# Kernel tuning notes

Measured on AMD Instinct MI355X. Metric: run time of the kernel, lower is better.

Reference implementation:

```python
import jax, jax.numpy as jnp
import numpy as np

B, H, S, E = 16384, 16, 1, 64
N_OTHERS = 4


def setup_inputs() -> dict:
    key = jax.random.key(0)
    ks = jax.random.split(key, N_OTHERS + 2)
    inp = {f"others_{i}": jax.random.normal(ks[i], (B, H, S, E), dtype=jnp.float32)
           for i in range(N_OTHERS)}
    inp["main"] = jax.random.normal(ks[N_OTHERS], (B, H, S, E), dtype=jnp.float32)
    inp["W"] = jax.random.normal(ks[N_OTHERS + 1], (E, E), dtype=jnp.float32) * (1.0 / np.sqrt(E))
    return inp


def reference(others_0, others_1, others_2, others_3, main, W):
    # mean over the 'others' modalities: (B, H, 1, E)
    mean = (others_0 + others_1 + others_2 + others_3) / 4.0
    m = jnp.squeeze(mean, 2)        # (B, H, E)
    main_sq = jnp.squeeze(main, 2)  # (B, H, E)
    # bilinear score: mean @ W @ main^T -> (B, H, H)
    score = jnp.einsum('bhe,ef,bgf->bhg', m, W, main_sq)
    attn = jax.nn.softmax(score, axis=-1)      # (B, H, H)
    context = jnp.einsum('bhg,bge->bhe', attn, main_sq)  # (B, H, E)
    return context, attn
```

## Files before the change

### kernel.cpp

```cpp
#include <hip/hip_runtime.h>

#define NBATCH 16384
#define H 16
#define E 64
#define NWAVE 4
#define NBLK (NBATCH / NWAVE)

typedef __attribute__((ext_vector_type(8))) short short8v;
typedef __attribute__((ext_vector_type(4))) float f32x4;

#define CFENCE asm volatile("" ::: "memory")

__device__ __forceinline__ unsigned short f2bf(float x) {
    return (unsigned short)(__float_as_uint(x) >> 16);
}
__device__ __forceinline__ float bfres(float x) {
    return x - __uint_as_float(__float_as_uint(x) & 0xFFFF0000u);
}

#define BSPLIT8(HIv, LOv, A, B) do { \
    HIv[0]=(short)f2bf(A.x); LOv[0]=(short)f2bf(bfres(A.x)); \
    HIv[1]=(short)f2bf(A.y); LOv[1]=(short)f2bf(bfres(A.y)); \
    HIv[2]=(short)f2bf(A.z); LOv[2]=(short)f2bf(bfres(A.z)); \
    HIv[3]=(short)f2bf(A.w); LOv[3]=(short)f2bf(bfres(A.w)); \
    HIv[4]=(short)f2bf(B.x); LOv[4]=(short)f2bf(bfres(B.x)); \
    HIv[5]=(short)f2bf(B.y); LOv[5]=(short)f2bf(bfres(B.y)); \
    HIv[6]=(short)f2bf(B.z); LOv[6]=(short)f2bf(bfres(B.z)); \
    HIv[7]=(short)f2bf(B.w); LOv[7]=(short)f2bf(bfres(B.w)); \
} while (0)

#define FMA4(ACC, S, B) do { \
    ACC.x = fmaf(S, B.x, ACC.x); ACC.y = fmaf(S, B.y, ACC.y); \
    ACC.z = fmaf(S, B.z, ACC.z); ACC.w = fmaf(S, B.w, ACC.w); } while (0)

#define SMAX1(X, OUT) do { \
    float mx_ = (X); \
    mx_ = fmaxf(mx_, __shfl_xor(mx_, 1)); \
    mx_ = fmaxf(mx_, __shfl_xor(mx_, 2)); \
    mx_ = fmaxf(mx_, __shfl_xor(mx_, 4)); \
    mx_ = fmaxf(mx_, __shfl_xor(mx_, 8)); \
    float e_ = __expf((X) - mx_); \
    float sm_ = e_; \
    sm_ += __shfl_xor(sm_, 1); \
    sm_ += __shfl_xor(sm_, 2); \
    sm_ += __shfl_xor(sm_, 4); \
    sm_ += __shfl_xor(sm_, 8); \
    OUT = e_ * __builtin_amdgcn_rcpf(sm_); \
} while (0)

__global__ __launch_bounds__(256) void w_frag_init(
    const float* __restrict__ W, unsigned short* __restrict__ wsW)
{
    const int flat = blockIdx.x * 256 + threadIdx.x;
    if (flat >= E * E) return;
    const float w = W[flat];
    const int e = flat >> 6, f = flat & 63;
    const int t = f >> 4, col = f & 15;
    const int s = e >> 5, khi = (e >> 3) & 3, i = e & 7;
    const int L = col + 16 * khi;
    wsW[((t * 2 + s) * 2 + 0) * 512 + L * 8 + i] = f2bf(w);
    wsW[((t * 2 + s) * 2 + 1) * 512 + L * 8 + i] = f2bf(bfres(w));
}

__global__ __launch_bounds__(256) void ovo_kernel(
    const float* __restrict__ o0, const float* __restrict__ o1,
    const float* __restrict__ o2, const float* __restrict__ o3,
    const float* __restrict__ mn, const unsigned short* __restrict__ wsW,
    float* __restrict__ ctx_out, float* __restrict__ attn_out)
{
    __shared__ float sT[NWAVE][2][H * 68];

    const int tid = threadIdx.x;
    const int l   = tid & 63;
    const int wv  = tid >> 6;
    const int r   = l & 15;
    const int q   = l >> 4;

    const int batch = blockIdx.x * NWAVE + wv;
    const size_t base = (size_t)batch * (H * E);

    float* const sU    = &sT[wv][0][0];
    float* const sMain = &sT[wv][1][0];

    float4 po0[4], po1[4], po2[4], po3[4];
#pragma unroll
    for (int sc = 0; sc < 4; ++sc) {
        const int s = sc >> 1, c01 = sc & 1;
        const size_t off = base + r * 64 + 32 * s + 8 * q + 4 * c01;
        po0[sc] = *(const float4*)(o0 + off);
        po1[sc] = *(const float4*)(o1 + off);
        po2[sc] = *(const float4*)(o2 + off);
        po3[sc] = *(const float4*)(o3 + off);
    }

    short8v ahi[2], alo[2];
#pragma unroll
    for (int s = 0; s < 2; ++s) {
        const int sa = s * 2, sb = s * 2 + 1;
        float4 mA, mB;
        mA.x = ((po0[sa].x + po1[sa].x) + (po2[sa].x + po3[sa].x)) * 0.25f;
        mA.y = ((po0[sa].y + po1[sa].y) + (po2[sa].y + po3[sa].y)) * 0.25f;
        mA.z = ((po0[sa].z + po1[sa].z) + (po2[sa].z + po3[sa].z)) * 0.25f;
        mA.w = ((po0[sa].w + po1[sa].w) + (po2[sa].w + po3[sa].w)) * 0.25f;
        mB.x = ((po0[sb].x + po1[sb].x) + (po2[sb].x + po3[sb].x)) * 0.25f;
        mB.y = ((po0[sb].y + po1[sb].y) + (po2[sb].y + po3[sb].y)) * 0.25f;
        mB.z = ((po0[sb].z + po1[sb].z) + (po2[sb].z + po3[sb].z)) * 0.25f;
        mB.w = ((po0[sb].w + po1[sb].w) + (po2[sb].w + po3[sb].w)) * 0.25f;
        BSPLIT8(ahi[s], alo[s], mA, mB);
    }

    float4 pmA, pmB, pmC, pmD;
    pmA = *(const float4*)(mn + base + r * 64 +      8 * q);
    pmB = *(const float4*)(mn + base + r * 64 +      8 * q + 4);
    pmC = *(const float4*)(mn + base + r * 64 + 32 + 8 * q);
    pmD = *(const float4*)(mn + base + r * 64 + 32 + 8 * q + 4);
    CFENCE;

#pragma unroll
    for (int t = 0; t < 4; ++t) {
        short8v bh0 = *(const short8v*)&wsW[((t * 2 + 0) * 2 + 0) * 512 + l * 8];
        short8v bl0 = *(const short8v*)&wsW[((t * 2 + 0) * 2 + 1) * 512 + l * 8];
        short8v bh1 = *(const short8v*)&wsW[((t * 2 + 1) * 2 + 0) * 512 + l * 8];
        short8v bl1 = *(const short8v*)&wsW[((t * 2 + 1) * 2 + 1) * 512 + l * 8];
        f32x4 acc = {0.f, 0.f, 0.f, 0.f};
        acc = __builtin_amdgcn_mfma_f32_16x16x32_bf16(ahi[0], bh0, acc, 0, 0, 0);
        acc = __builtin_amdgcn_mfma_f32_16x16x32_bf16(alo[0], bh0, acc, 0, 0, 0);
        acc = __builtin_amdgcn_mfma_f32_16x16x32_bf16(ahi[0], bl0, acc, 0, 0, 0);
        acc = __builtin_amdgcn_mfma_f32_16x16x32_bf16(ahi[1], bh1, acc, 0, 0, 0);
        acc = __builtin_amdgcn_mfma_f32_16x16x32_bf16(alo[1], bh1, acc, 0, 0, 0);
        acc = __builtin_amdgcn_mfma_f32_16x16x32_bf16(ahi[1], bl1, acc, 0, 0, 0);
#pragma unroll
        for (int j = 0; j < 4; ++j)
            sU[(4 * q + j) * 68 + 16 * t + r] = acc[j];
    }

    *(float4*)&sMain[r * 68 +      8 * q]     = pmA;
    *(float4*)&sMain[r * 68 +      8 * q + 4] = pmB;
    *(float4*)&sMain[r * 68 + 32 + 8 * q]     = pmC;
    *(float4*)&sMain[r * 68 + 32 + 8 * q + 4] = pmD;
    CFENCE;

    f32x4 d3 = {0.f, 0.f, 0.f, 0.f};
    {
        float4 a01 = *(const float4*)&sU[r * 68 + 8 * q];
        float4 a23 = *(const float4*)&sU[r * 68 + 8 * q + 4];
        short8v ah, al2, bh, bl2;
        BSPLIT8(ah, al2, a01, a23);
        BSPLIT8(bh, bl2, pmA, pmB);
        d3 = __builtin_amdgcn_mfma_f32_16x16x32_bf16(ah,  bh,  d3, 0, 0, 0);
        d3 = __builtin_amdgcn_mfma_f32_16x16x32_bf16(al2, bh,  d3, 0, 0, 0);
        d3 = __builtin_amdgcn_mfma_f32_16x16x32_bf16(ah,  bl2, d3, 0, 0, 0);
    }
    {
        float4 a01 = *(const float4*)&sU[r * 68 + 32 + 8 * q];
        float4 a23 = *(const float4*)&sU[r * 68 + 32 + 8 * q + 4];
        short8v ah, al2, bh, bl2;
        BSPLIT8(ah, al2, a01, a23);
        BSPLIT8(bh, bl2, pmC, pmD);
        d3 = __builtin_amdgcn_mfma_f32_16x16x32_bf16(ah,  bh,  d3, 0, 0, 0);
        d3 = __builtin_amdgcn_mfma_f32_16x16x32_bf16(al2, bh,  d3, 0, 0, 0);
        d3 = __builtin_amdgcn_mfma_f32_16x16x32_bf16(ah,  bl2, d3, 0, 0, 0);
    }
    CFENCE;

    float4 at4;
    SMAX1(d3[0], at4.x);
    SMAX1(d3[1], at4.y);
    SMAX1(d3[2], at4.z);
    SMAX1(d3[3], at4.w);
    *(float4*)&sU[r * 20 + 4 * q] = at4;
    {
        float* ap = attn_out + (size_t)batch * (H * H);
        ap[(4 * q + 0) * 16 + r] = at4.x;
        ap[(4 * q + 1) * 16 + r] = at4.y;
        ap[(4 * q + 2) * 16 + r] = at4.z;
        ap[(4 * q + 3) * 16 + r] = at4.w;
    }
    CFENCE;

    {
        const int h0 = q * 4, e0c = r * 4;
        float4 c0 = {0.f,0.f,0.f,0.f}, c1 = {0.f,0.f,0.f,0.f};
        float4 c2 = {0.f,0.f,0.f,0.f}, c3 = {0.f,0.f,0.f,0.f};
#pragma unroll
        for (int g = 0; g < 16; ++g) {
            float4 bvv = *(const float4*)&sMain[g * 68 + e0c];
            float4 avv = *(const float4*)&sU[g * 20 + h0];
            FMA4(c0, avv.x, bvv);
            FMA4(c1, avv.y, bvv);
            FMA4(c2, avv.z, bvv);
            FMA4(c3, avv.w, bvv);
        }
        float* cp = ctx_out + base;
        *(float4*)(cp + (h0 + 0) * 64 + e0c) = c0;
        *(float4*)(cp + (h0 + 1) * 64 + e0c) = c1;
        *(float4*)(cp + (h0 + 2) * 64 + e0c) = c2;
        *(float4*)(cp + (h0 + 3) * 64 + e0c) = c3;
    }
}

extern "C" void kernel_launch(void* const* d_in, const int* in_sizes, int n_in,
                              void* d_out, int out_size, void* d_ws, size_t ws_size,
                              hipStream_t stream) {
    const float* o0 = (const float*)d_in[0];
    const float* o1 = (const float*)d_in[1];
    const float* o2 = (const float*)d_in[2];
    const float* o3 = (const float*)d_in[3];
    const float* mn = (const float*)d_in[4];
    const float* W  = (const float*)d_in[5];
    float* ctx  = (float*)d_out;
    float* attn = ctx + (size_t)NBATCH * H * E;
    unsigned short* wsW = (unsigned short*)d_ws;

    hipLaunchKernelGGL(w_frag_init, dim3(16), dim3(256), 0, stream, W, wsW);
    hipLaunchKernelGGL(ovo_kernel, dim3(NBLK), dim3(256), 0, stream,
                       o0, o1, o2, o3, mn, wsW, ctx, attn);
}
```

Measured before the change: 97.97 us.

## Use single-wave blocks looping over batches with software-prefetched next-batch loads

Measured after the change: 96.36 us. About the same (-1.6%).

```diff
diff --git a/kernel.cpp b/kernel.cpp
--- a/kernel.cpp
+++ b/kernel.cpp
@@ -3,8 +3,8 @@
 #define NBATCH 16384
 #define H 16
 #define E 64
-#define NWAVE 4
-#define NBLK (NBATCH / NWAVE)
+#define NB 4
+#define NBLK (NBATCH / NB)
 
 typedef __attribute__((ext_vector_type(8))) short short8v;
 typedef __attribute__((ext_vector_type(4))) float f32x4;
@@ -62,140 +62,161 @@
     wsW[((t * 2 + s) * 2 + 1) * 512 + L * 8 + i] = f2bf(bfres(w));
 }
 
-__global__ __launch_bounds__(256) void ovo_kernel(
+__global__ __launch_bounds__(64, 1) void ovo_kernel(
     const float* __restrict__ o0, const float* __restrict__ o1,
     const float* __restrict__ o2, const float* __restrict__ o3,
     const float* __restrict__ mn, const unsigned short* __restrict__ wsW,
     float* __restrict__ ctx_out, float* __restrict__ attn_out)
 {
-    __shared__ float sT[NWAVE][2][H * 68];
-
-    const int tid = threadIdx.x;
-    const int l   = tid & 63;
-    const int wv  = tid >> 6;
-    const int r   = l & 15;
-    const int q   = l >> 4;
-
-    const int batch = blockIdx.x * NWAVE + wv;
-    const size_t base = (size_t)batch * (H * E);
-
-    float* const sU    = &sT[wv][0][0];
-    float* const sMain = &sT[wv][1][0];
+    __shared__ float sU[H * 68];
+    __shared__ float sMain[H * 68];
+
+    const int l = threadIdx.x;
+    const int r = l & 15;
+    const int q = l >> 4;
+    const int bid = blockIdx.x;
 
     float4 po0[4], po1[4], po2[4], po3[4];
-#pragma unroll
-    for (int sc = 0; sc < 4; ++sc) {
-        const int s = sc >> 1, c01 = sc & 1;
-        const size_t off = base + r * 64 + 32 * s + 8 * q + 4 * c01;
-        po0[sc] = *(const float4*)(o0 + off);
-        po1[sc] = *(const float4*)(o1 + off);
-        po2[sc] = *(const float4*)(o2 + off);
-        po3[sc] = *(const float4*)(o3 + off);
+    float4 pmA, pmB, pmC, pmD;
+    {
+        const size_t base = (size_t)bid * (H * E);
+#pragma unroll
+        for (int sc = 0; sc < 4; ++sc) {
+            const int s = sc >> 1, c01 = sc & 1;
+            const size_t off = base + r * 64 + 32 * s + 8 * q + 4 * c01;
+            po0[sc] = *(const float4*)(o0 + off);
+            po1[sc] = *(const float4*)(o1 + off);
+            po2[sc] = *(const float4*)(o2 + off);
+            po3[sc] = *(const float4*)(o3 + off);
+        }
+        pmA = *(const float4*)(mn + base + r * 64 +      8 * q);
+        pmB = *(const float4*)(mn + base + r * 64 +      8 * q + 4);
+        pmC = *(const float4*)(mn + base + r * 64 + 32 + 8 * q);
+        pmD = *(const float4*)(mn + base + r * 64 + 32 + 8 * q + 4);
     }
 
-    short8v ahi[2], alo[2];
-#pragma unroll
-    for (int s = 0; s < 2; ++s) {
-        const int sa = s * 2, sb = s * 2 + 1;
-        float4 mA, mB;
-        mA.x = ((po0[sa].x + po1[sa].x) + (po2[sa].x + po3[sa].x)) * 0.25f;
-        mA.y = ((po0[sa].y + po1[sa].y) + (po2[sa].y + po3[sa].y)) * 0.25f;
-        mA.z = ((po0[sa].z + po1[sa].z) + (po2[sa].z + po3[sa].z)) * 0.25f;
-        mA.w = ((po0[sa].w + po1[sa].w) + (po2[sa].w + po3[sa].w)) * 0.25f;
-        mB.x = ((po0[sb].x + po1[sb].x) + (po2[sb].x + po3[sb].x)) * 0.25f;
-        mB.y = ((po0[sb].y + po1[sb].y) + (po2[sb].y + po3[sb].y)) * 0.25f;
-        mB.z = ((po0[sb].z + po1[sb].z) + (po2[sb].z + po3[sb].z)) * 0.25f;
-        mB.w = ((po0[sb].w + po1[sb].w) + (po2[sb].w + po3[sb].w)) * 0.25f;
-        BSPLIT8(ahi[s], alo[s], mA, mB);
-    }
-
-    float4 pmA, pmB, pmC, pmD;
-    pmA = *(const float4*)(mn + base + r * 64 +      8 * q);
-    pmB = *(const float4*)(mn + base + r * 64 +      8 * q + 4);
-    pmC = *(const float4*)(mn + base + r * 64 + 32 + 8 * q);
-    pmD = *(const float4*)(mn + base + r * 64 + 32 + 8 * q + 4);
-    CFENCE;
-
-#pragma unroll
-    for (int t = 0; t < 4; ++t) {
-        short8v bh0 = *(const short8v*)&wsW[((t * 2 + 0) * 2 + 0) * 512 + l * 8];
-        short8v bl0 = *(const short8v*)&wsW[((t * 2 + 0) * 2 + 1) * 512 + l * 8];
-        short8v bh1 = *(const short8v*)&wsW[((t * 2 + 1) * 2 + 0) * 512 + l * 8];
-        short8v bl1 = *(const short8v*)&wsW[((t * 2 + 1) * 2 + 1) * 512 + l * 8];
-        f32x4 acc = {0.f, 0.f, 0.f, 0.f};
-        acc = __builtin_amdgcn_mfma_f32_16x16x32_bf16(ahi[0], bh0, acc, 0, 0, 0);
-        acc = __builtin_amdgcn_mfma_f32_16x16x32_bf16(alo[0], bh0, acc, 0, 0, 0);
-        acc = __builtin_amdgcn_mfma_f32_16x16x32_bf16(ahi[0], bl0, acc, 0, 0, 0);
-        acc = __builtin_amdgcn_mfma_f32_16x16x32_bf16(ahi[1], bh1, acc, 0, 0, 0);
-        acc = __builtin_amdgcn_mfma_f32_16x16x32_bf16(alo[1], bh1, acc, 0, 0, 0);
-        acc = __builtin_amdgcn_mfma_f32_16x16x32_bf16(ahi[1], bl1, acc, 0, 0, 0);
-#pragma unroll
-        for (int j = 0; j < 4; ++j)
-            sU[(4 * q + j) * 68 + 16 * t + r] = acc[j];
-    }
-
-    *(float4*)&sMain[r * 68 +      8 * q]     = pmA;
-    *(float4*)&sMain[r * 68 +      8 * q + 4] = pmB;
-    *(float4*)&sMain[r * 68 + 32 + 8 * q]     = pmC;
-    *(float4*)&sMain[r * 68 + 32 + 8 * q + 4] = pmD;
-    CFENCE;
-
-    f32x4 d3 = {0.f, 0.f, 0.f, 0.f};
-    {
-        float4 a01 = *(const float4*)&sU[r * 68 + 8 * q];
-        float4 a23 = *(const float4*)&sU[r * 68 + 8 * q + 4];
-        short8v ah, al2, bh, bl2;
-        BSPLIT8(ah, al2, a01, a23);
-        BSPLIT8(bh, bl2, pmA, pmB);
-        d3 = __builtin_amdgcn_mfma_f32_16x16x32_bf16(ah,  bh,  d3, 0, 0, 0);
-        d3 = __builtin_amdgcn_mfma_f32_16x16x32_bf16(al2, bh,  d3, 0, 0, 0);
-        d3 = __builtin_amdgcn_mfma_f32_16x16x32_bf16(ah,  bl2, d3, 0, 0, 0);
-    }
-    {
-        float4 a01 = *(const float4*)&sU[r * 68 + 32 + 8 * q];
-        float4 a23 = *(const float4*)&sU[r * 68 + 32 + 8 * q + 4];
-        short8v ah, al2, bh, bl2;
-        BSPLIT8(ah, al2, a01, a23);
-        BSPLIT8(bh, bl2, pmC, pmD);
-        d3 = __builtin_amdgcn_mfma_f32_16x16x32_bf16(ah,  bh,  d3, 0, 0, 0);
-        d3 = __builtin_amdgcn_mfma_f32_16x16x32_bf16(al2, bh,  d3, 0, 0, 0);
-        d3 = __builtin_amdgcn_mfma_f32_16x16x32_bf16(ah,  bl2, d3, 0, 0, 0);
-    }
-    CFENCE;
-
-    float4 at4;
-    SMAX1(d3[0], at4.x);
-    SMAX1(d3[1], at4.y);
-    SMAX1(d3[2], at4.z);
-    SMAX1(d3[3], at4.w);
-    *(float4*)&sU[r * 20 + 4 * q] = at4;
-    {
-        float* ap = attn_out + (size_t)batch * (H * H);
-        ap[(4 * q + 0) * 16 + r] = at4.x;
-        ap[(4 * q + 1) * 16 + r] = at4.y;
-        ap[(4 * q + 2) * 16 + r] = at4.z;
-        ap[(4 * q + 3) * 16 + r] = at4.w;
-    }
-    CFENCE;
-
-    {
-        const int h0 = q * 4, e0c = r * 4;
-        float4 c0 = {0.f,0.f,0.f,0.f}, c1 = {0.f,0.f,0.f,0.f};
-        float4 c2 = {0.f,0.f,0.f,0.f}, c3 = {0.f,0.f,0.f,0.f};
-#pragma unroll
-        for (int g = 0; g < 16; ++g) {
-            float4 bvv = *(const float4*)&sMain[g * 68 + e0c];
-            float4 avv = *(const float4*)&sU[g * 20 + h0];
-            FMA4(c0, avv.x, bvv);
-            FMA4(c1, avv.y, bvv);
-            FMA4(c2, avv.z, bvv);
-            FMA4(c3, avv.w, bvv);
-        }
-        float* cp = ctx_out + base;
-        *(float4*)(cp + (h0 + 0) * 64 + e0c) = c0;
-        *(float4*)(cp + (h0 + 1) * 64 + e0c) = c1;
-        *(float4*)(cp + (h0 + 2) * 64 + e0c) = c2;
-        *(float4*)(cp + (h0 + 3) * 64 + e0c) = c3;
+#pragma unroll 1
+    for (int it = 0; it < NB; ++it) {
+        const int batch = it * NBLK + bid;
+        const size_t base = (size_t)batch * (H * E);
+
+        short8v ahi[2], alo[2];
+#pragma unroll
+        for (int s = 0; s < 2; ++s) {
+            const int sa = s * 2, sb = s * 2 + 1;
+            float4 mA, mB;
+            mA.x = ((po0[sa].x + po1[sa].x) + (po2[sa].x + po3[sa].x)) * 0.25f;
+            mA.y = ((po0[sa].y + po1[sa].y) + (po2[sa].y + po3[sa].y)) * 0.25f;
+            mA.z = ((po0[sa].z + po1[sa].z) + (po2[sa].z + po3[sa].z)) * 0.25f;
+            mA.w = ((po0[sa].w + po1[sa].w) + (po2[sa].w + po3[sa].w)) * 0.25f;
+            mB.x = ((po0[sb].x + po1[sb].x) + (po2[sb].x + po3[sb].x)) * 0.25f;
+            mB.y = ((po0[sb].y + po1[sb].y) + (po2[sb].y + po3[sb].y)) * 0.25f;
+            mB.z = ((po0[sb].z + po1[sb].z) + (po2[sb].z + po3[sb].z)) * 0.25f;
+            mB.w = ((po0[sb].w + po1[sb].w) + (po2[sb].w + po3[sb].w)) * 0.25f;
+            BSPLIT8(ahi[s], alo[s], mA, mB);
+        }
+        CFENCE;
+
+#pragma unroll
+        for (int t = 0; t < 4; ++t) {
+            short8v bh0 = *(const short8v*)&wsW[((t * 2 + 0) * 2 + 0) * 512 + l * 8];
+            short8v bl0 = *(const short8v*)&wsW[((t * 2 + 0) * 2 + 1) * 512 + l * 8];
+            short8v bh1 = *(const short8v*)&wsW[((t * 2 + 1) * 2 + 0) * 512 + l * 8];
+            short8v bl1 = *(const short8v*)&wsW[((t * 2 + 1) * 2 + 1) * 512 + l * 8];
+            f32x4 acc = {0.f, 0.f, 0.f, 0.f};
+            acc = __builtin_amdgcn_mfma_f32_16x16x32_bf16(ahi[0], bh0, acc, 0, 0, 0);
+            acc = __builtin_amdgcn_mfma_f32_16x16x32_bf16(alo[0], bh0, acc, 0, 0, 0);
+            acc = __builtin_amdgcn_mfma_f32_16x16x32_bf16(ahi[0], bl0, acc, 0, 0, 0);
+            acc = __builtin_amdgcn_mfma_f32_16x16x32_bf16(ahi[1], bh1, acc, 0, 0, 0);
+            acc = __builtin_amdgcn_mfma_f32_16x16x32_bf16(alo[1], bh1, acc, 0, 0, 0);
+            acc = __builtin_amdgcn_mfma_f32_16x16x32_bf16(ahi[1], bl1, acc, 0, 0, 0);
+#pragma unroll
+            for (int j = 0; j < 4; ++j)
+                sU[(4 * q + j) * 68 + 16 * t + r] = acc[j];
+        }
+
+        *(float4*)&sMain[r * 68 +      8 * q]     = pmA;
+        *(float4*)&sMain[r * 68 +      8 * q + 4] = pmB;
+        *(float4*)&sMain[r * 68 + 32 + 8 * q]     = pmC;
+        *(float4*)&sMain[r * 68 + 32 + 8 * q + 4] = pmD;
+        CFENCE;
+
+        f32x4 d3 = {0.f, 0.f, 0.f, 0.f};
+        {
+            float4 a01 = *(const float4*)&sU[r * 68 + 8 * q];
+            float4 a23 = *(const float4*)&sU[r * 68 + 8 * q + 4];
+            short8v ah, al2, bh, bl2;
+            BSPLIT8(ah, al2, a01, a23);
+            BSPLIT8(bh, bl2, pmA, pmB);
+            d3 = __builtin_amdgcn_mfma_f32_16x16x32_bf16(ah,  bh,  d3, 0, 0, 0);
+            d3 = __builtin_amdgcn_mfma_f32_16x16x32_bf16(al2, bh,  d3, 0, 0, 0);
+            d3 = __builtin_amdgcn_mfma_f32_16x16x32_bf16(ah,  bl2, d3, 0, 0, 0);
+        }
+        {
+            float4 a01 = *(const float4*)&sU[r * 68 + 32 + 8 * q];
+            float4 a23 = *(const float4*)&sU[r * 68 + 32 + 8 * q + 4];
+            short8v ah, al2, bh, bl2;
+            BSPLIT8(ah, al2, a01, a23);
+            BSPLIT8(bh, bl2, pmC, pmD);
+            d3 = __builtin_amdgcn_mfma_f32_16x16x32_bf16(ah,  bh,  d3, 0, 0, 0);
+            d3 = __builtin_amdgcn_mfma_f32_16x16x32_bf16(al2, bh,  d3, 0, 0, 0);
+            d3 = __builtin_amdgcn_mfma_f32_16x16x32_bf16(ah,  bl2, d3, 0, 0, 0);
+        }
+        CFENCE;
+
+        if (it + 1 < NB) {
+            const size_t nbase = base + (size_t)NBLK * (H * E);
+#pragma unroll
+            for (int sc = 0; sc < 4; ++sc) {
+                const int s = sc >> 1, c01 = sc & 1;
+                const size_t off = nbase + r * 64 + 32 * s + 8 * q + 4 * c01;
+                po0[sc] = *(const float4*)(o0 + off);
+                po1[sc] = *(const float4*)(o1 + off);
+                po2[sc] = *(const float4*)(o2 + off);
+                po3[sc] = *(const float4*)(o3 + off);
+            }
+            pmA = *(const float4*)(mn + nbase + r * 64 +      8 * q);
+            pmB = *(const float4*)(mn + nbase + r * 64 +      8 * q + 4);
+            pmC = *(const float4*)(mn + nbase + r * 64 + 32 + 8 * q);
+            pmD = *(const float4*)(mn + nbase + r * 64 + 32 + 8 * q + 4);
+        }
+        CFENCE;
+
+        float4 at4;
+        SMAX1(d3[0], at4.x);
+        SMAX1(d3[1], at4.y);
+        SMAX1(d3[2], at4.z);
+        SMAX1(d3[3], at4.w);
+        *(float4*)&sU[r * 20 + 4 * q] = at4;
+        {
+            float* ap = attn_out + (size_t)batch * (H * H);
+            ap[(4 * q + 0) * 16 + r] = at4.x;
+            ap[(4 * q + 1) * 16 + r] = at4.y;
+            ap[(4 * q + 2) * 16 + r] = at4.z;
+            ap[(4 * q + 3) * 16 + r] = at4.w;
+        }
+        CFENCE;
+
+        {
+            const int h0 = q * 4, e0c = r * 4;
+            float4 c0 = {0.f,0.f,0.f,0.f}, c1 = {0.f,0.f,0.f,0.f};
+            float4 c2 = {0.f,0.f,0.f,0.f}, c3 = {0.f,0.f,0.f,0.f};
+#pragma unroll
+            for (int g = 0; g < 16; ++g) {
+                float4 bvv = *(const float4*)&sMain[g * 68 + e0c];
+                float4 avv = *(const float4*)&sU[g * 20 + h0];
+                FMA4(c0, avv.x, bvv);
+                FMA4(c1, avv.y, bvv);
+                FMA4(c2, avv.z, bvv);
+                FMA4(c3, avv.w, bvv);
+            }
+            float* cp = ctx_out + base;
+            *(float4*)(cp + (h0 + 0) * 64 + e0c) = c0;
+            *(float4*)(cp + (h0 + 1) * 64 + e0c) = c1;
+            *(float4*)(cp + (h0 + 2) * 64 + e0c) = c2;
+            *(float4*)(cp + (h0 + 3) * 64 + e0c) = c3;
+        }
+        CFENCE;
     }
 }
 
@@ -213,6 +234,6 @@
     unsigned short* wsW = (unsigned short*)d_ws;
 
     hipLaunchKernelGGL(w_frag_init, dim3(16), dim3(256), 0, stream, W, wsW);
-    hipLaunchKernelGGL(ovo_kernel, dim3(NBLK), dim3(256), 0, stream,
+    hipLaunchKernelGGL(ovo_kernel, dim3(NBLK), dim3(64), 0, stream,
                        o0, o1, o2, o3, mn, wsW, ctx, attn);
 }
```
